# Kernel tuning notes

Measured on AMD Instinct MI355X. Metric: run time of the kernel, lower is better.

The kernel has to match this reference:

```python
import jax, jax.numpy as jnp
import numpy as np

WS = 3          # windows_size
ND = 3          # num_dilation, dilations [1,2,3]
NSTATE = 16     # d_state
RANK = 12       # dt_rank = ceil(192/16)
TOPK = 36       # max(1,(20//3)**2)*depth
DM = 192        # d_model
DI = 384        # d_inner = 2*d_model
B0, HH, WW = 8, 96, 96


def setup_inputs() -> dict:
    ks = jax.random.split(jax.random.key(0), 12)
    f = jax.random.normal
    return {
        "x": f(ks[0], (B0, HH, WW, DM), jnp.float32),
        "W_in": f(ks[1], (2 * DI, DM), jnp.float32) * 0.02,
        "conv_w": f(ks[2], (DI, 1, 7, 7), jnp.float32) * 0.05,
        "conv_b": f(ks[3], (DI,), jnp.float32) * 0.01,
        "x_proj_w": f(ks[4], (2, RANK + 2 * NSTATE, DI), jnp.float32) * 0.02,
        "dt_w": f(ks[5], (2, DI, RANK), jnp.float32) * 0.02,
        "dt_b": f(ks[6], (2, DI), jnp.float32) * 0.01,
        "A_logs": jnp.tile(jnp.log(jnp.arange(1, NSTATE + 1, dtype=jnp.float32)), (2 * DI, 1)),
        "Ds": jnp.ones((2 * DI,), jnp.float32),
        "W_kv": f(ks[7], (2 * DI, DI), jnp.float32) * 0.02,
        "b_kv": jnp.zeros((2 * DI,), jnp.float32),
        "ln_g": jnp.ones((DI,), jnp.float32),
        "ln_b": jnp.zeros((DI,), jnp.float32),
        "W_out": f(ks[8], (DM, DI), jnp.float32) * 0.02,
    }


def _selective_scan(xs, x_proj_w, dt_w, dt_b, A_logs, Ds):
    # xs: (B, K=2, D, L) -> (B, K, D, L). Standard Mamba selective scan.
    B, K, D, L = xs.shape
    x_dbl = jnp.einsum('bkdl,kcd->bkcl', xs, x_proj_w)          # (B,K,R+2N,L)
    dts = x_dbl[:, :, :RANK]
    Bs = x_dbl[:, :, RANK:RANK + NSTATE]                        # (B,K,N,L)
    Cs = x_dbl[:, :, RANK + NSTATE:]                            # (B,K,N,L)
    delta = jax.nn.softplus(jnp.einsum('bkrl,kdr->bkdl', dts, dt_w) + dt_b[None, :, :, None])
    A = -jnp.exp(A_logs).reshape(K, D, NSTATE)
    dA = jnp.exp(delta[..., None] * A[None, :, :, None, :])    # (B,K,D,L,N)
    dBu = delta[..., None] * Bs.transpose(0, 1, 3, 2)[:, :, None, :, :] * xs[..., None]
    dA = jnp.moveaxis(dA, 3, 0)                                 # (L,B,K,D,N)
    dBu = jnp.moveaxis(dBu, 3, 0)
    C = jnp.moveaxis(Cs, 3, 0)                                  # (L,B,K,N)

    def step(h, inp):
        dA_t, dBu_t, C_t = inp
        h = dA_t * h + dBu_t
        y = jnp.einsum('bkdn,bkn->bkd', h, C_t)
        return h, y

    h0 = jnp.zeros((B, K, D, NSTATE), xs.dtype)
    _, ys = jax.lax.scan(step, h0, (dA, dBu, C))                # ys: (L,B,K,D)
    y = jnp.moveaxis(ys, 0, 3)                                  # (B,K,D,L)
    return y + Ds.reshape(1, K, D, 1) * xs


def _dynamic_mask_active(x):
    # x: (B,D,H,W). Partition into WSxWS windows, keep TOPK by mean activation.
    B, D, H, W = x.shape
    nH, nW = H // WS, W // WS
    w = x.reshape(B, D, nH, WS, nW, WS).transpose(0, 2, 4, 1, 3, 5)
    w = w.reshape(B, nH * nW, D, WS * WS)                       # (B,nWin,D,ws2)
    score = w.mean(axis=(2, 3))                                 # (B,nWin)
    _, idx = jax.lax.top_k(score, TOPK)                         # (B,TOPK)
    g = jnp.take_along_axis(w, idx[:, :, None, None], axis=1)   # (B,TOPK,D,ws2)
    return g.transpose(0, 2, 1, 3).reshape(B, D, TOPK * WS * WS)


def _unfold(x, d):
    # torch nn.Unfold(kernel=WS, dilation=d, padding=d, stride=1) on (B,C,H,W)
    B, C, H, W = x.shape
    xp = jnp.pad(x, ((0, 0), (0, 0), (d, d), (d, d)))
    pats = [xp[:, :, i * d:i * d + H, j * d:j * d + W] for i in range(WS) for j in range(WS)]
    p = jnp.stack(pats, axis=2)                                 # (B,C,ws2,H,W) channel-major like torch
    return p.reshape(B, C, WS * WS, H * W)


def _forward(x, W_in, conv_w, conv_b, x_proj_w, dt_w, dt_b, A_logs, Ds,
             W_kv, b_kv, ln_g, ln_b, W_out):
    B, H, W_, _ = x.shape
    xz = jnp.einsum('bhwc,oc->bhwo', x, W_in)
    xf, z = jnp.split(xz, 2, axis=-1)                           # (B,H,W,DI) each
    xc = xf.transpose(0, 3, 1, 2)
    xc = jax.lax.conv_general_dilated(xc, conv_w, (1, 1), [(3, 3), (3, 3)],
                                      feature_group_count=conv_w.shape[0],
                                      dimension_numbers=('NCHW', 'OIHW', 'NCHW'))
    xc = xc + conv_b[None, :, None, None]                       # (B,DI,H,W)
    D = xc.shape[1]

    # foreground SSM on active windows (forward + flipped scan)
    act = _dynamic_mask_active(xc)                              # (B,D,L)
    xs = jnp.stack([act, jnp.flip(act, axis=-1)], axis=1)       # (B,2,D,L)
    out = _selective_scan(xs, x_proj_w, dt_w, dt_b, A_logs, Ds)
    y1 = out[:, 0] + jnp.flip(out[:, 1], axis=-1)               # (B,D,L)
    y1 = y1.transpose(0, 2, 1)                                  # (B,L,D)

    L = y1.shape[1]
    ws2 = WS * WS
    n2 = L // ws2
    kv = jnp.einsum('bld,od->blo', y1, W_kv) + b_kv             # (B,L,2D)
    hd = 2 * D // ND
    t = kv.reshape(B, n2, ws2, ND, hd).transpose(3, 0, 4, 2, 1)  # (ND,B,hd,ws2,n2)
    Q, Kt = t[:, :, :hd // 2], t[:, :, hd // 2:]                 # (ND,B,D/ND,ws2,n2)

    dch = D // ND
    xr = xc.reshape(B, ND, dch, H, W_)
    ys = []
    for i in range(ND):
        V = _unfold(xr[:, i], i + 1)                            # (B,dch,ws2,n1)
        V = V.transpose(0, 1, 3, 2)                             # (B,dch,n1,ws2)
        s = jnp.einsum('bcwn,bcwn->bcw', Q[i], Kt[i]) / np.sqrt(dch).astype(np.float32)
        # softmax over a singleton axis (as in the source) -> all ones
        A_M = jax.nn.softmax(s[..., None], axis=-1)[..., 0]     # (B,dch,ws2)
        ys.append(jnp.einsum('bcnw,bcw->bcn', V, A_M))          # (B,dch,n1)
    y = jnp.concatenate(ys, axis=1)                             # (B,D,n1)
    y = y.transpose(0, 2, 1)                                    # (B,n1,D)

    mu = y.mean(-1, keepdims=True)
    var = y.var(-1, keepdims=True)
    y = (y - mu) / jnp.sqrt(var + 1e-5) * ln_g + ln_b
    y = y.reshape(B, H, W_, D) + z
    return jnp.einsum('bhwd,od->bhwo', y, W_out)


def reference(x, W_in, conv_w, conv_b, x_proj_w, dt_w, dt_b, A_logs, Ds,
              W_kv, b_kv, ln_g, ln_b, W_out):
    return _forward(x, W_in, conv_w, conv_b, x_proj_w, dt_w, dt_b, A_logs, Ds,
                    W_kv, b_kv, ln_g, ln_b, W_out)
```

## Files before the change

kernel.cpp:

```cpp
#include <hip/hip_runtime.h>
#include <cstddef>

#define B0V 8
#define HSV 96
#define WSV 96
#define DMV 192
#define DIV 384
#define MTOT (B0V*HSV*WSV)

typedef __attribute__((ext_vector_type(8))) unsigned short ushort8v;
typedef __attribute__((ext_vector_type(8))) short short8v;
typedef __attribute__((ext_vector_type(4))) float f32x4;
typedef _Float16 h2 __attribute__((ext_vector_type(2)));
typedef _Float16 h8 __attribute__((ext_vector_type(8)));

__device__ __forceinline__ unsigned short f2bf(float f) {
    unsigned int i; __builtin_memcpy(&i, &f, 4);
    i += 0x7FFFu + ((i >> 16) & 1);
    return (unsigned short)(i >> 16);
}

template<int ROWS>
__device__ __forceinline__ void stageBF16(const unsigned short* __restrict__ src, int ld,
                                          unsigned short* lds, int t) {
#pragma unroll
    for (int i = 0; i < ROWS*8/256; ++i) {
        const int cid = t + i*256;
        const int r = cid >> 3, cb = cid & 7;
        ushort8v sv = *(const ushort8v*)(src + (size_t)r*ld + cb*8);
        *(ushort8v*)((char*)lds + r*128 + ((cb ^ (r&7))<<4)) = sv;
    }
}
__device__ __forceinline__ short8v fragRead(const unsigned short* lds, int row, int kchunk) {
    return *(const short8v*)((const char*)lds + row*128 + ((kchunk ^ (row&7))<<4));
}

__global__ __launch_bounds__(192) void wc_kernel(
    const float* __restrict__ Wout, const float* __restrict__ Win,
    unsigned short* __restrict__ Wch)
{
    const int o = blockIdx.x;
    const int c = threadIdx.x;
    __shared__ float wrow[384];
    for (int j = threadIdx.x; j < 384; j += 192) wrow[j] = Wout[(size_t)o*384 + j];
    __syncthreads();
    float acc = 0.f;
#pragma unroll 4
    for (int j = 0; j < 384; ++j)
        acc += wrow[j] * Win[(size_t)(384 + j)*192 + c];
    Wch[(size_t)o*192 + c] = f2bf(acc);
}

__global__ __launch_bounds__(256) void wprep_kernel(
    const float* __restrict__ cw, h2* __restrict__ w2h)
{
    const int idx = blockIdx.x*256 + threadIdx.x;
    if (idx < 49*192) {
        const int tap = idx / 192, cp = idx % 192;
        h2 v;
        v[0] = (_Float16)cw[(size_t)(2*cp  )*49 + tap];
        v[1] = (_Float16)cw[(size_t)(2*cp+1)*49 + tap];
        w2h[idx] = v;
    }
}

__global__ __launch_bounds__(256) void cvt_kernel(
    const float* __restrict__ src, unsigned short* __restrict__ dst, int n8)
{
    const int i = blockIdx.x*256 + threadIdx.x;
    if (i < n8) {
        const float4 f0 = *(const float4*)(src + (size_t)i*8);
        const float4 f1 = *(const float4*)(src + (size_t)i*8 + 4);
        ushort8v v;
        v[0]=f2bf(f0.x); v[1]=f2bf(f0.y); v[2]=f2bf(f0.z); v[3]=f2bf(f0.w);
        v[4]=f2bf(f1.x); v[5]=f2bf(f1.y); v[6]=f2bf(f1.z); v[7]=f2bf(f1.w);
        *(ushort8v*)(dst + (size_t)i*8) = v;
    }
}

__global__ __launch_bounds__(256) void gemm_in_mfma(
    const float* __restrict__ x, const unsigned short* __restrict__ Wh,
    unsigned short* __restrict__ xh, _Float16* __restrict__ xf)
{
    __shared__ unsigned short As[3*128*64];
    __shared__ unsigned short Bs[128*64];
    const int t = threadIdx.x;
    const int m0 = blockIdx.x * 128;
    const int wid = t >> 6, lane = t & 63;
    const int wm = wid >> 1, wn = wid & 1;
    const int li = lane & 15, lg = lane >> 4;

#pragma unroll
    for (int kb = 0; kb < 3; ++kb) {
#pragma unroll
        for (int i = 0; i < 4; ++i) {
            const int cid = t + i*256;
            const int r = cid >> 3, cb = cid & 7;
            const float* p = x + (size_t)(m0 + r)*DMV + kb*64 + cb*8;
            float4 f0 = *(const float4*)p;
            float4 f1 = *(const float4*)(p+4);
            ushort8v sv;
            sv[0]=f2bf(f0.x); sv[1]=f2bf(f0.y); sv[2]=f2bf(f0.z); sv[3]=f2bf(f0.w);
            sv[4]=f2bf(f1.x); sv[5]=f2bf(f1.y); sv[6]=f2bf(f1.z); sv[7]=f2bf(f1.w);
            *(ushort8v*)((char*)(As + kb*128*64) + r*128 + ((cb ^ (r&7))<<4)) = sv;
            *(ushort8v*)(xh + (size_t)(m0 + r)*DMV + kb*64 + cb*8) = sv;
        }
    }

    for (int n0i = 0; n0i < 3; ++n0i) {
        const int n0 = n0i * 128;
        f32x4 acc[4][4];
#pragma unroll
        for (int i = 0; i < 4; ++i)
#pragma unroll
            for (int j = 0; j < 4; ++j) acc[i][j] = (f32x4){0.f,0.f,0.f,0.f};

        for (int kb = 0; kb < 3; ++kb) {
            __syncthreads();
            stageBF16<128>(Wh + (size_t)n0*DMV + kb*64, DMV, Bs, t);
            __syncthreads();
#pragma unroll
            for (int ks = 0; ks < 2; ++ks) {
                short8v a[4], b[4];
#pragma unroll
                for (int mf = 0; mf < 4; ++mf)
                    a[mf] = fragRead(As + kb*128*64, wm*64 + mf*16 + li, ks*4 + lg);
#pragma unroll
                for (int nf = 0; nf < 4; ++nf)
                    b[nf] = fragRead(Bs, wn*64 + nf*16 + li, ks*4 + lg);
#pragma unroll
                for (int mf = 0; mf < 4; ++mf)
#pragma unroll
                    for (int nf = 0; nf < 4; ++nf)
                        acc[mf][nf] = __builtin_amdgcn_mfma_f32_16x16x32_bf16(a[mf], b[nf], acc[mf][nf], 0, 0, 0);
            }
        }
#pragma unroll
        for (int mf = 0; mf < 4; ++mf)
#pragma unroll
            for (int nf = 0; nf < 4; ++nf)
#pragma unroll
                for (int i = 0; i < 4; ++i) {
                    const int row = m0 + wm*64 + mf*16 + lg*4 + i;
                    const int col = n0 + wn*64 + nf*16 + li;
                    xf[(size_t)row*DIV + col] = (_Float16)acc[mf][nf][i];
                }
    }
}

__global__ __launch_bounds__(256) void dwconv_kernel(
    const _Float16* __restrict__ xf, const h2* __restrict__ w2h,
    const float* __restrict__ cb, _Float16* __restrict__ xc)
{
    const int tile = blockIdx.x;
    const int th = tile / 6, tw = tile % 6;
    const int h0 = th*8, w0 = tw*16;
    const int c0 = blockIdx.y*64, b = blockIdx.z;

    __shared__ _Float16 patch[14*22*64];
    const int t = threadIdx.x;
    for (int idx = t; idx < 308*8; idx += 256) {
        const int sp = idx >> 3, c8 = idx & 7;
        const int ih = sp / 22, iw = sp - ih*22;
        const int gh = h0 - 3 + ih, gw = w0 - 3 + iw;
        ushort8v v;
#pragma unroll
        for (int j = 0; j < 8; ++j) v[j] = 0;
        if ((unsigned)gh < (unsigned)HSV && (unsigned)gw < (unsigned)WSV)
            v = *(const ushort8v*)(xf + (((size_t)b*HSV + gh)*WSV + gw)*DIV + c0 + c8*8);
        *(ushort8v*)(patch + sp*64 + c8*8) = v;
    }
    __syncthreads();

    const int cp = t & 31;
    const int wq = t >> 5;

    h2 wreg[49];
    const h2* wp = w2h + (c0 >> 1) + cp;
#pragma unroll
    for (int k = 0; k < 49; ++k) wreg[k] = wp[k*192];

    h2 biasv;
    biasv[0] = (_Float16)cb[c0 + 2*cp];
    biasv[1] = (_Float16)cb[c0 + 2*cp + 1];
    h2 acc[8][2];
#pragma unroll
    for (int i = 0; i < 8; ++i) { acc[i][0] = biasv; acc[i][1] = biasv; }

    const h2* prow = (const h2*)patch;
#pragma unroll
    for (int ih = 0; ih < 14; ++ih) {
        h2 r[8];
#pragma unroll
        for (int j = 0; j < 8; ++j)
            r[j] = prow[(ih*22 + wq*2 + j)*32 + cp];
#pragma unroll
        for (int kw = 0; kw < 7; ++kw) {
#pragma unroll
            for (int oh = 0; oh < 8; ++oh) {
                const int kh = ih - oh;
                if (kh >= 0 && kh < 7) {
                    acc[oh][0] += wreg[kh*7 + kw] * r[kw];
                    acc[oh][1] += wreg[kh*7 + kw] * r[kw + 1];
                }
            }
        }
    }
    h2* xcp = (h2*)xc;
#pragma unroll
    for (int oh = 0; oh < 8; ++oh)
#pragma unroll
        for (int j = 0; j < 2; ++j)
            xcp[((((size_t)b*HSV + h0+oh)*WSV + (w0 + wq*2 + j))*DIV + c0)/2 + cp] = acc[oh][j];
}

__global__ __launch_bounds__(256) void boxln_kernel(
    const _Float16* __restrict__ xc,
    const float* __restrict__ g, const float* __restrict__ bta,
    unsigned short* __restrict__ yln)
{
    const int wid  = threadIdx.x >> 6;
    const int lane = threadIdx.x & 63;
    const int m = blockIdx.x * 4 + wid;
    const int b  = m / (HSV*WSV);
    const int hw = m % (HSV*WSV);
    const int h = hw / WSV, w = hw % WSV;

    const bool act = lane < 48;
    const int ch = lane * 8;
    const int dd = (ch >> 7) + 1;

    float s[8];
#pragma unroll
    for (int j = 0; j < 8; ++j) s[j] = 0.f;

#pragma unroll
    for (int a = -1; a <= 1; ++a)
#pragma unroll
        for (int bb = -1; bb <= 1; ++bb) {
            const int h2_ = h + a*dd, w2_ = w + bb*dd;
            if (act && (unsigned)h2_ < (unsigned)HSV && (unsigned)w2_ < (unsigned)WSV) {
                h8 v = *(const h8*)(xc + (((size_t)b*HSV + h2_)*WSV + w2_)*DIV + ch);
#pragma unroll
                for (int j = 0; j < 8; ++j) s[j] += (float)v[j];
            }
        }

    float ps = 0.f, ps2 = 0.f;
#pragma unroll
    for (int j = 0; j < 8; ++j) { ps += s[j]; ps2 += s[j]*s[j]; }
#pragma unroll
    for (int off = 32; off > 0; off >>= 1) {
        ps  += __shfl_xor(ps,  off);
        ps2 += __shfl_xor(ps2, off);
    }
    const float mu   = ps * (1.f/384.f);
    const float var  = ps2 * (1.f/384.f) - mu*mu;
    const float rstd = rsqrtf(var + 1e-5f);

    if (act) {
        float4 g0 = *(const float4*)(g + ch);
        float4 g1 = *(const float4*)(g + ch + 4);
        float4 b0 = *(const float4*)(bta + ch);
        float4 b1 = *(const float4*)(bta + ch + 4);
        float gv[8] = {g0.x,g0.y,g0.z,g0.w,g1.x,g1.y,g1.z,g1.w};
        float bv[8] = {b0.x,b0.y,b0.z,b0.w,b1.x,b1.y,b1.z,b1.w};
        ushort8v o;
#pragma unroll
        for (int j = 0; j < 8; ++j)
            o[j] = f2bf((s[j] - mu)*rstd*gv[j] + bv[j]);
        *(ushort8v*)(yln + (size_t)m*DIV + ch) = o;
    }
}

__global__ __launch_bounds__(256) void gemm_out_mfma(
    const unsigned short* __restrict__ Yl, const unsigned short* __restrict__ WoutH,
    const unsigned short* __restrict__ xh, const unsigned short* __restrict__ Wch,
    float* __restrict__ out)
{
    __shared__ unsigned short As[128*64];
    __shared__ unsigned short Bs[192*64];
    const int t = threadIdx.x;
    const int m0 = blockIdx.x * 128;
    const int wid = t >> 6, lane = t & 63;
    const int wm = wid >> 1, wn = wid & 1;
    const int li = lane & 15, lg = lane >> 4;

    f32x4 acc[4][6];
#pragma unroll
    for (int i = 0; i < 4; ++i)
#pragma unroll
        for (int j = 0; j < 6; ++j) acc[i][j] = (f32x4){0.f,0.f,0.f,0.f};

    for (int kb = 0; kb < 9; ++kb) {
        if (kb < 6) {
            stageBF16<128>(Yl + (size_t)m0*DIV + kb*64, DIV, As, t);
            stageBF16<192>(WoutH + kb*64, DIV, Bs, t);
        } else {
            stageBF16<128>(xh + (size_t)m0*DMV + (kb-6)*64, DMV, As, t);
            stageBF16<192>(Wch + (kb-6)*64, DMV, Bs, t);
        }
        __syncthreads();
#pragma unroll
        for (int ks = 0; ks < 2; ++ks) {
            short8v a[4], b[6];
#pragma unroll
            for (int mf = 0; mf < 4; ++mf) a[mf] = fragRead(As, wm*64 + mf*16 + li, ks*4 + lg);
#pragma unroll
            for (int nf = 0; nf < 6; ++nf) b[nf] = fragRead(Bs, wn*96 + nf*16 + li, ks*4 + lg);
#pragma unroll
            for (int mf = 0; mf < 4; ++mf)
#pragma unroll
                for (int nf = 0; nf < 6; ++nf)
                    acc[mf][nf] = __builtin_amdgcn_mfma_f32_16x16x32_bf16(a[mf], b[nf], acc[mf][nf], 0, 0, 0);
        }
        __syncthreads();
    }
#pragma unroll
    for (int mf = 0; mf < 4; ++mf)
#pragma unroll
        for (int nf = 0; nf < 6; ++nf)
#pragma unroll
            for (int i = 0; i < 4; ++i) {
                const int row = m0 + wm*64 + mf*16 + lg*4 + i;
                const int col = wn*96 + nf*16 + li;
                out[(size_t)row*DMV + col] = acc[mf][nf][i];
            }
}

extern "C" void kernel_launch(void* const* d_in, const int* in_sizes, int n_in,
                              void* d_out, int out_size, void* d_ws, size_t ws_size,
                              hipStream_t stream)
{
    const float* x      = (const float*)d_in[0];
    const float* W_in   = (const float*)d_in[1];
    const float* conv_w = (const float*)d_in[2];
    const float* conv_b = (const float*)d_in[3];
    const float* ln_g   = (const float*)d_in[11];
    const float* ln_b   = (const float*)d_in[12];
    const float* W_out  = (const float*)d_in[13];
    float* out = (float*)d_out;

    char* ws = (char*)d_ws;
    unsigned short* Wch   = (unsigned short*)(ws);
    h2*             w2h   = (h2*)(ws + 0x20000);
    unsigned short* WinfH = (unsigned short*)(ws + 0x40000);
    unsigned short* WoutH = (unsigned short*)(ws + 0x80000);
    unsigned short* xh    = (unsigned short*)(ws + 0x100000);
    _Float16*       xf    = (_Float16*)(ws + 0x2000000);
    _Float16*       xc    = (_Float16*)d_out;

    wc_kernel    <<<dim3(192),          192, 0, stream>>>(W_out, W_in, Wch);
    wprep_kernel <<<dim3(37),           256, 0, stream>>>(conv_w, w2h);
    cvt_kernel   <<<dim3(36),           256, 0, stream>>>(W_in,  WinfH, 384*192/8);
    cvt_kernel   <<<dim3(36),           256, 0, stream>>>(W_out, WoutH, 192*384/8);
    gemm_in_mfma <<<dim3(MTOT/128),     256, 0, stream>>>(x, WinfH, xh, xf);
    dwconv_kernel<<<dim3(72, 6, B0V),   256, 0, stream>>>(xf, w2h, conv_b, xc);
    boxln_kernel <<<dim3(MTOT/4),       256, 0, stream>>>(xc, ln_g, ln_b,
                                                          (unsigned short*)xf);
    gemm_out_mfma<<<dim3(MTOT/128),     256, 0, stream>>>((const unsigned short*)xf,
                                                          WoutH, xh, Wch, out);
}
```

Baseline: 207.0 us.

## Fuse weight-prep kernels, halve GEMM M-tiles, and swizzle dwconv block order

Four small weight-preparation launches are merged into one prep kernel that dispatches by block index, saving three launches. Both MFMA GEMMs shrink their M tile from 128 to 64 rows, with the four waves split along N instead of a 2x2 grid. This doubles the grid size for better occupancy and CU coverage, at the cost of less reuse of the staged weight tile per block. The depthwise conv grid is flattened to 1D with an id swizzle that spreads consecutive blocks across batches, presumably to balance load across XCDs or L2.

```diff
diff --git a/kernel.cpp b/kernel.cpp
--- a/kernel.cpp
+++ b/kernel.cpp
@@ -35,46 +35,54 @@
     return *(const short8v*)((const char*)lds + row*128 + ((kchunk ^ (row&7))<<4));
 }
 
-__global__ __launch_bounds__(192) void wc_kernel(
+__global__ __launch_bounds__(256) void prep_kernel(
     const float* __restrict__ Wout, const float* __restrict__ Win,
-    unsigned short* __restrict__ Wch)
-{
-    const int o = blockIdx.x;
-    const int c = threadIdx.x;
-    __shared__ float wrow[384];
-    for (int j = threadIdx.x; j < 384; j += 192) wrow[j] = Wout[(size_t)o*384 + j];
-    __syncthreads();
-    float acc = 0.f;
+    const float* __restrict__ cw,
+    unsigned short* __restrict__ Wch, h2* __restrict__ w2h,
+    unsigned short* __restrict__ WinfH, unsigned short* __restrict__ WoutH)
+{
+    const int blk = blockIdx.x;
+    const int t = threadIdx.x;
+    if (blk < 192) {
+        __shared__ float wrow[384];
+        for (int j = t; j < 384; j += 256) wrow[j] = Wout[(size_t)blk*384 + j];
+        __syncthreads();
+        if (t < 192) {
+            float acc = 0.f;
 #pragma unroll 4
-    for (int j = 0; j < 384; ++j)
-        acc += wrow[j] * Win[(size_t)(384 + j)*192 + c];
-    Wch[(size_t)o*192 + c] = f2bf(acc);
-}
-
-__global__ __launch_bounds__(256) void wprep_kernel(
-    const float* __restrict__ cw, h2* __restrict__ w2h)
-{
-    const int idx = blockIdx.x*256 + threadIdx.x;
-    if (idx < 49*192) {
-        const int tap = idx / 192, cp = idx % 192;
-        h2 v;
-        v[0] = (_Float16)cw[(size_t)(2*cp  )*49 + tap];
-        v[1] = (_Float16)cw[(size_t)(2*cp+1)*49 + tap];
-        w2h[idx] = v;
-    }
-}
-
-__global__ __launch_bounds__(256) void cvt_kernel(
-    const float* __restrict__ src, unsigned short* __restrict__ dst, int n8)
-{
-    const int i = blockIdx.x*256 + threadIdx.x;
-    if (i < n8) {
-        const float4 f0 = *(const float4*)(src + (size_t)i*8);
-        const float4 f1 = *(const float4*)(src + (size_t)i*8 + 4);
-        ushort8v v;
-        v[0]=f2bf(f0.x); v[1]=f2bf(f0.y); v[2]=f2bf(f0.z); v[3]=f2bf(f0.w);
-        v[4]=f2bf(f1.x); v[5]=f2bf(f1.y); v[6]=f2bf(f1.z); v[7]=f2bf(f1.w);
-        *(ushort8v*)(dst + (size_t)i*8) = v;
+            for (int j = 0; j < 384; ++j)
+                acc += wrow[j] * Win[(size_t)(384 + j)*192 + t];
+            Wch[(size_t)blk*192 + t] = f2bf(acc);
+        }
+    } else if (blk < 229) {
+        const int idx = (blk - 192)*256 + t;
+        if (idx < 49*192) {
+            const int tap = idx / 192, cp = idx % 192;
+            h2 v;
+            v[0] = (_Float16)cw[(size_t)(2*cp  )*49 + tap];
+            v[1] = (_Float16)cw[(size_t)(2*cp+1)*49 + tap];
+            w2h[idx] = v;
+        }
+    } else if (blk < 265) {
+        const int i = (blk - 229)*256 + t;
+        if (i < 384*192/8) {
+            const float4 f0 = *(const float4*)(Win + (size_t)i*8);
+            const float4 f1 = *(const float4*)(Win + (size_t)i*8 + 4);
+            ushort8v v;
+            v[0]=f2bf(f0.x); v[1]=f2bf(f0.y); v[2]=f2bf(f0.z); v[3]=f2bf(f0.w);
+            v[4]=f2bf(f1.x); v[5]=f2bf(f1.y); v[6]=f2bf(f1.z); v[7]=f2bf(f1.w);
+            *(ushort8v*)(WinfH + (size_t)i*8) = v;
+        }
+    } else {
+        const int i = (blk - 265)*256 + t;
+        if (i < 192*384/8) {
+            const float4 f0 = *(const float4*)(Wout + (size_t)i*8);
+            const float4 f1 = *(const float4*)(Wout + (size_t)i*8 + 4);
+            ushort8v v;
+            v[0]=f2bf(f0.x); v[1]=f2bf(f0.y); v[2]=f2bf(f0.z); v[3]=f2bf(f0.w);
+            v[4]=f2bf(f1.x); v[5]=f2bf(f1.y); v[6]=f2bf(f1.z); v[7]=f2bf(f1.w);
+            *(ushort8v*)(WoutH + (size_t)i*8) = v;
+        }
     }
 }
 
@@ -82,18 +90,17 @@
     const float* __restrict__ x, const unsigned short* __restrict__ Wh,
     unsigned short* __restrict__ xh, _Float16* __restrict__ xf)
 {
-    __shared__ unsigned short As[3*128*64];
+    __shared__ unsigned short As[3*64*64];
     __shared__ unsigned short Bs[128*64];
     const int t = threadIdx.x;
-    const int m0 = blockIdx.x * 128;
+    const int m0 = blockIdx.x * 64;
     const int wid = t >> 6, lane = t & 63;
-    const int wm = wid >> 1, wn = wid & 1;
     const int li = lane & 15, lg = lane >> 4;
 
 #pragma unroll
     for (int kb = 0; kb < 3; ++kb) {
 #pragma unroll
-        for (int i = 0; i < 4; ++i) {
+        for (int i = 0; i < 2; ++i) {
             const int cid = t + i*256;
             const int r = cid >> 3, cb = cid & 7;
             const float* p = x + (size_t)(m0 + r)*DMV + kb*64 + cb*8;
@@ -102,18 +109,18 @@
             ushort8v sv;
             sv[0]=f2bf(f0.x); sv[1]=f2bf(f0.y); sv[2]=f2bf(f0.z); sv[3]=f2bf(f0.w);
             sv[4]=f2bf(f1.x); sv[5]=f2bf(f1.y); sv[6]=f2bf(f1.z); sv[7]=f2bf(f1.w);
-            *(ushort8v*)((char*)(As + kb*128*64) + r*128 + ((cb ^ (r&7))<<4)) = sv;
+            *(ushort8v*)((char*)(As + kb*64*64) + r*128 + ((cb ^ (r&7))<<4)) = sv;
             *(ushort8v*)(xh + (size_t)(m0 + r)*DMV + kb*64 + cb*8) = sv;
         }
     }
 
     for (int n0i = 0; n0i < 3; ++n0i) {
         const int n0 = n0i * 128;
-        f32x4 acc[4][4];
+        f32x4 acc[4][2];
 #pragma unroll
         for (int i = 0; i < 4; ++i)
 #pragma unroll
-            for (int j = 0; j < 4; ++j) acc[i][j] = (f32x4){0.f,0.f,0.f,0.f};
+            for (int j = 0; j < 2; ++j) acc[i][j] = (f32x4){0.f,0.f,0.f,0.f};
 
         for (int kb = 0; kb < 3; ++kb) {
             __syncthreads();
@@ -121,28 +128,28 @@
             __syncthreads();
 #pragma unroll
             for (int ks = 0; ks < 2; ++ks) {
-                short8v a[4], b[4];
+                short8v a[4], b[2];
 #pragma unroll
                 for (int mf = 0; mf < 4; ++mf)
-                    a[mf] = fragRead(As + kb*128*64, wm*64 + mf*16 + li, ks*4 + lg);
-#pragma unroll
-                for (int nf = 0; nf < 4; ++nf)
-                    b[nf] = fragRead(Bs, wn*64 + nf*16 + li, ks*4 + lg);
+                    a[mf] = fragRead(As + kb*64*64, mf*16 + li, ks*4 + lg);
+#pragma unroll
+                for (int nf = 0; nf < 2; ++nf)
+                    b[nf] = fragRead(Bs, wid*32 + nf*16 + li, ks*4 + lg);
 #pragma unroll
                 for (int mf = 0; mf < 4; ++mf)
 #pragma unroll
-                    for (int nf = 0; nf < 4; ++nf)
+                    for (int nf = 0; nf < 2; ++nf)
                         acc[mf][nf] = __builtin_amdgcn_mfma_f32_16x16x32_bf16(a[mf], b[nf], acc[mf][nf], 0, 0, 0);
             }
         }
 #pragma unroll
         for (int mf = 0; mf < 4; ++mf)
 #pragma unroll
-            for (int nf = 0; nf < 4; ++nf)
+            for (int nf = 0; nf < 2; ++nf)
 #pragma unroll
                 for (int i = 0; i < 4; ++i) {
-                    const int row = m0 + wm*64 + mf*16 + lg*4 + i;
-                    const int col = n0 + wn*64 + nf*16 + li;
+                    const int row = m0 + mf*16 + lg*4 + i;
+                    const int col = n0 + wid*32 + nf*16 + li;
                     xf[(size_t)row*DIV + col] = (_Float16)acc[mf][nf][i];
                 }
     }
@@ -152,10 +159,15 @@
     const _Float16* __restrict__ xf, const h2* __restrict__ w2h,
     const float* __restrict__ cb, _Float16* __restrict__ xc)
 {
-    const int tile = blockIdx.x;
+    const int id  = blockIdx.x;
+    const int swz = (id & 7) * 432 + (id >> 3);
+    const int b    = swz / 432;
+    const int rem  = swz - b*432;
+    const int cg   = rem / 72;
+    const int tile = rem - cg*72;
     const int th = tile / 6, tw = tile % 6;
     const int h0 = th*8, w0 = tw*16;
-    const int c0 = blockIdx.y*64, b = blockIdx.z;
+    const int c0 = cg*64;
 
     __shared__ _Float16 patch[14*22*64];
     const int t = threadIdx.x;
@@ -278,40 +290,39 @@
     const unsigned short* __restrict__ xh, const unsigned short* __restrict__ Wch,
     float* __restrict__ out)
 {
-    __shared__ unsigned short As[128*64];
+    __shared__ unsigned short As[64*64];
     __shared__ unsigned short Bs[192*64];
     const int t = threadIdx.x;
-    const int m0 = blockIdx.x * 128;
+    const int m0 = blockIdx.x * 64;
     const int wid = t >> 6, lane = t & 63;
-    const int wm = wid >> 1, wn = wid & 1;
     const int li = lane & 15, lg = lane >> 4;
 
-    f32x4 acc[4][6];
+    f32x4 acc[4][3];
 #pragma unroll
     for (int i = 0; i < 4; ++i)
 #pragma unroll
-        for (int j = 0; j < 6; ++j) acc[i][j] = (f32x4){0.f,0.f,0.f,0.f};
+        for (int j = 0; j < 3; ++j) acc[i][j] = (f32x4){0.f,0.f,0.f,0.f};
 
     for (int kb = 0; kb < 9; ++kb) {
         if (kb < 6) {
-            stageBF16<128>(Yl + (size_t)m0*DIV + kb*64, DIV, As, t);
+            stageBF16<64> (Yl + (size_t)m0*DIV + kb*64, DIV, As, t);
             stageBF16<192>(WoutH + kb*64, DIV, Bs, t);
         } else {
-            stageBF16<128>(xh + (size_t)m0*DMV + (kb-6)*64, DMV, As, t);
+            stageBF16<64> (xh + (size_t)m0*DMV + (kb-6)*64, DMV, As, t);
             stageBF16<192>(Wch + (kb-6)*64, DMV, Bs, t);
         }
         __syncthreads();
 #pragma unroll
         for (int ks = 0; ks < 2; ++ks) {
-            short8v a[4], b[6];
-#pragma unroll
-            for (int mf = 0; mf < 4; ++mf) a[mf] = fragRead(As, wm*64 + mf*16 + li, ks*4 + lg);
-#pragma unroll
-            for (int nf = 0; nf < 6; ++nf) b[nf] = fragRead(Bs, wn*96 + nf*16 + li, ks*4 + lg);
+            short8v a[4], b[3];
+#pragma unroll
+            for (int mf = 0; mf < 4; ++mf) a[mf] = fragRead(As, mf*16 + li, ks*4 + lg);
+#pragma unroll
+            for (int nf = 0; nf < 3; ++nf) b[nf] = fragRead(Bs, wid*48 + nf*16 + li, ks*4 + lg);
 #pragma unroll
             for (int mf = 0; mf < 4; ++mf)
 #pragma unroll
-                for (int nf = 0; nf < 6; ++nf)
+                for (int nf = 0; nf < 3; ++nf)
                     acc[mf][nf] = __builtin_amdgcn_mfma_f32_16x16x32_bf16(a[mf], b[nf], acc[mf][nf], 0, 0, 0);
         }
         __syncthreads();
@@ -319,11 +330,11 @@
 #pragma unroll
     for (int mf = 0; mf < 4; ++mf)
 #pragma unroll
-        for (int nf = 0; nf < 6; ++nf)
+        for (int nf = 0; nf < 3; ++nf)
 #pragma unroll
             for (int i = 0; i < 4; ++i) {
-                const int row = m0 + wm*64 + mf*16 + lg*4 + i;
-                const int col = wn*96 + nf*16 + li;
+                const int row = m0 + mf*16 + lg*4 + i;
+                const int col = wid*48 + nf*16 + li;
                 out[(size_t)row*DMV + col] = acc[mf][nf][i];
             }
 }
@@ -350,14 +361,12 @@
     _Float16*       xf    = (_Float16*)(ws + 0x2000000);
     _Float16*       xc    = (_Float16*)d_out;
 
-    wc_kernel    <<<dim3(192),          192, 0, stream>>>(W_out, W_in, Wch);
-    wprep_kernel <<<dim3(37),           256, 0, stream>>>(conv_w, w2h);
-    cvt_kernel   <<<dim3(36),           256, 0, stream>>>(W_in,  WinfH, 384*192/8);
-    cvt_kernel   <<<dim3(36),           256, 0, stream>>>(W_out, WoutH, 192*384/8);
-    gemm_in_mfma <<<dim3(MTOT/128),     256, 0, stream>>>(x, WinfH, xh, xf);
-    dwconv_kernel<<<dim3(72, 6, B0V),   256, 0, stream>>>(xf, w2h, conv_b, xc);
+    prep_kernel  <<<dim3(301),          256, 0, stream>>>(W_out, W_in, conv_w,
+                                                          Wch, w2h, WinfH, WoutH);
+    gemm_in_mfma <<<dim3(MTOT/64),      256, 0, stream>>>(x, WinfH, xh, xf);
+    dwconv_kernel<<<dim3(3456),         256, 0, stream>>>(xf, w2h, conv_b, xc);
     boxln_kernel <<<dim3(MTOT/4),       256, 0, stream>>>(xc, ln_g, ln_b,
                                                           (unsigned short*)xf);
-    gemm_out_mfma<<<dim3(MTOT/128),     256, 0, stream>>>((const unsigned short*)xf,
+    gemm_out_mfma<<<dim3(MTOT/64),      256, 0, stream>>>((const unsigned short*)xf,
                                                           WoutH, xh, Wch, out);
 }
```

Result: no change. 206.9 us (-0.1%).
